# Kernel optimization log

Measured on AMD Instinct MI355X. Metric: run time of the kernel, lower is better.

## Reference

```python
import jax, jax.numpy as jnp
import numpy as np

N, D_IN, D_ATTN = 8192, 48, 8


def setup_inputs() -> dict:
    key = jax.random.key(0)
    ks = jax.random.split(key, 9)
    s = 1.0 / np.sqrt(D_IN)
    return {
        "x": jax.random.normal(ks[0], (N, D_IN), jnp.float32),
        "Kw": jax.random.normal(ks[1], (D_IN, D_ATTN), jnp.float32) * s,
        "Kb": jax.random.normal(ks[2], (D_ATTN,), jnp.float32) * s,
        "Qw": jax.random.normal(ks[3], (D_IN, D_ATTN), jnp.float32) * s,
        "Qb": jax.random.normal(ks[4], (D_ATTN,), jnp.float32) * s,
        "Vw": jax.random.normal(ks[5], (D_IN, D_ATTN), jnp.float32) * s,
        "Vb": jax.random.normal(ks[6], (D_ATTN,), jnp.float32) * s,
        "Zw": jax.random.normal(ks[7], (D_ATTN, D_IN), jnp.float32) * (1.0 / np.sqrt(D_ATTN)),
        "Zb": jax.random.normal(ks[8], (D_IN,), jnp.float32) * (1.0 / np.sqrt(D_ATTN)),
    }


def reference(x, Kw, Kb, Qw, Qb, Vw, Vb, Zw, Zb):
    # Tiny QKV projections: [N,48] -> [N,8]
    Xk = x @ Kw + Kb
    Xq = x @ Qw + Qb
    Xv = x @ Vw + Vb
    # Attention over the batch/row dimension: [N,8]@[8,N] -> [N,N]
    scale = jnp.sqrt(jnp.asarray(D_ATTN, jnp.float32))
    AM = jax.nn.softmax(Xk @ Xq.T / scale, axis=1)  # torch F.softmax 2D default dim=1
    Z = AM @ Xv                                      # [N,8]
    return x + (Z @ Zw + Zb)                         # residual + output proj [N,48]
```

## Files before the change

kernel.cpp:

```cpp
#include <hip/hip_runtime.h>
#include <hip/hip_fp16.h>


#define XKS_OFF  0
#define Q4_OFF   32768
#define VT_OFF   65536
#define KN2_OFF  102400
#define BMAX_OFF 110592
#define PART_OFF 110848

typedef _Float16 half8 __attribute__((ext_vector_type(8)));
typedef float f32x16 __attribute__((ext_vector_type(16)));
union U8 { unsigned u[4]; half8 h; };

static __device__ __forceinline__ unsigned pku(float a, float b) {
    auto t = __builtin_amdgcn_cvt_pkrtz(a, b);
    union { decltype(t) x; unsigned u; } c; c.x = t; return c.u;
}

__global__ __launch_bounds__(256) void proj_kernel(
    const float* __restrict__ x,
    const float* __restrict__ Kw, const float* __restrict__ Kb,
    const float* __restrict__ Qw, const float* __restrict__ Qb,
    const float* __restrict__ Vw, const float* __restrict__ Vb,
    unsigned* __restrict__ Xksf16, unsigned* __restrict__ Q4,
    unsigned* __restrict__ Vt, float* __restrict__ kn2,
    float* __restrict__ bmax)
{
    __shared__ float xs[32 * 49];
    __shared__ float wAll[3 * 388];
    __shared__ float bs[24];
    __shared__ float outv[32][25];
    const int tid = threadIdx.x;
    const int r0 = blockIdx.x * 32;

    for (int i = tid; i < 1536; i += 256) {
        int r = i / 48, c = i - r * 48;
        xs[r * 49 + c] = x[r0 * 48 + i];
    }
    for (int i = tid; i < 384; i += 256) {
        wAll[i]       = Kw[i];
        wAll[388 + i] = Qw[i];
        wAll[776 + i] = Vw[i];
    }
    if (tid < 8)       bs[tid] = Kb[tid];
    else if (tid < 16) bs[tid] = Qb[tid - 8];
    else if (tid < 24) bs[tid] = Vb[tid - 16];
    __syncthreads();

    const int rl = tid >> 3;
    const int g  = tid & 7;
    const int c0 = 3 * g;
    const float* xr = &xs[rl * 49];
    const float* w0 = &wAll[((c0 + 0) >> 3) * 388 + ((c0 + 0) & 7)];
    const float* w1 = &wAll[((c0 + 1) >> 3) * 388 + ((c0 + 1) & 7)];
    const float* w2 = &wAll[((c0 + 2) >> 3) * 388 + ((c0 + 2) & 7)];
    float a0 = bs[c0], a1 = bs[c0 + 1], a2 = bs[c0 + 2];
    #pragma unroll
    for (int k = 0; k < 48; k++) {
        const float xv = xr[k];
        a0 = fmaf(xv, w0[k * 8], a0);
        a1 = fmaf(xv, w1[k * 8], a1);
        a2 = fmaf(xv, w2[k * 8], a2);
    }
    outv[rl][c0] = a0; outv[rl][c0 + 1] = a1; outv[rl][c0 + 2] = a2;
    __syncthreads();

    const float kscale = 0.51008732149f;
    if (tid < 32) {
        uint4 o;
        o.x = pku(outv[tid][0] * kscale, outv[tid][1] * kscale);
        o.y = pku(outv[tid][2] * kscale, outv[tid][3] * kscale);
        o.z = pku(outv[tid][4] * kscale, outv[tid][5] * kscale);
        o.w = pku(outv[tid][6] * kscale, outv[tid][7] * kscale);
        ((uint4*)Xksf16)[r0 + tid] = o;
    } else if (tid < 64) {
        const int r = tid - 32;
        uint4 o;
        o.x = pku(outv[r][8],  outv[r][9]);
        o.y = pku(outv[r][10], outv[r][11]);
        o.z = pku(outv[r][12], outv[r][13]);
        o.w = pku(outv[r][14], outv[r][15]);
        ((uint4*)Q4)[r0 + r] = o;
    } else if (tid < 192) {
        const int i = tid - 64;
        const int c = i >> 4, t = i & 15;
        Vt[c * 4096 + blockIdx.x * 16 + t] =
            pku(outv[2 * t][16 + c], outv[2 * t + 1][16 + c]);
    } else if (tid < 224) {
        const int r = tid - 192;
        float n2 = 0.f;
        #pragma unroll
        for (int c = 0; c < 8; c++) n2 = fmaf(outv[r][8 + c], outv[r][8 + c], n2);
        #pragma unroll
        for (int off = 16; off > 0; off >>= 1)
            n2 = fmaxf(n2, __shfl_xor(n2, off, 64));
        if (r == 0) bmax[blockIdx.x] = n2;
    } else {
        const int r = tid - 224;
        float s = 0.f;
        #pragma unroll
        for (int c = 0; c < 8; c++) { const float v = outv[r][c]; s = fmaf(v, v, s); }
        kn2[r0 + r] = s * (kscale * kscale);
    }
    if (tid < 16)
        Vt[8 * 4096 + blockIdx.x * 16 + tid] = 0x3C003C00u;
}

__global__ __launch_bounds__(256) void attn_kernel(
    const uint4* __restrict__ Xks4, const uint4* __restrict__ Q4,
    const unsigned* __restrict__ Vt, const float* __restrict__ kn2,
    const float* __restrict__ bmax, float* __restrict__ part, int ntiles)
{
    const int tid  = threadIdx.x;
    const int lane = tid & 63;
    const int wv   = tid >> 6;
    const int wid  = blockIdx.x * 4 + wv;
    const int rg = wid & 255, ch = wid >> 8;
    const int h = lane >> 5, hl = lane & 31;
    const int rbase = rg * 32;
    const int j0base = ch * (ntiles * 32);

    float m = fmaxf(fmaxf(bmax[lane], bmax[64 + lane]),
                    fmaxf(bmax[128 + lane], bmax[192 + lane]));
    #pragma unroll
    for (int off = 32; off > 0; off >>= 1)
        m = fmaxf(m, __shfl_xor(m, off, 64));
    const float qmax2 = m;

    U8 Bk;
    if (h == 0) {
        const uint4 kv = Xks4[rbase + hl];
        Bk.u[0] = kv.x; Bk.u[1] = kv.y; Bk.u[2] = kv.z; Bk.u[3] = kv.w;
    } else {
        const float sinit = -sqrtf(kn2[rbase + hl] * qmax2);
        Bk.u[0] = pku(sinit, 0.f); Bk.u[1] = 0u; Bk.u[2] = 0u; Bk.u[3] = 0u;
    }

    const f32x16 zc = {0.f,0.f,0.f,0.f,0.f,0.f,0.f,0.f,
                       0.f,0.f,0.f,0.f,0.f,0.f,0.f,0.f};
    f32x16 acc = {0.f,0.f,0.f,0.f,0.f,0.f,0.f,0.f,
                  0.f,0.f,0.f,0.f,0.f,0.f,0.f,0.f};

    const int cva = hl < 9 ? hl : 8;
    const uint2* V2 = (const uint2*)Vt;
    const int u2base = cva * 2048 + h;

    int j0 = j0base;
    uint4 qv_n  = Q4[j0 + hl];
    uint2 va0_n = V2[u2base + (j0 >> 2) + 0];
    uint2 va1_n = V2[u2base + (j0 >> 2) + 2];
    uint2 va2_n = V2[u2base + (j0 >> 2) + 4];
    uint2 va3_n = V2[u2base + (j0 >> 2) + 6];

    for (int t = 0; t < ntiles; ++t) {
        const uint4 qv  = qv_n;
        const uint2 va0 = va0_n, va1 = va1_n, va2 = va2_n, va3 = va3_n;
        if (t + 1 < ntiles) {
            const int j1 = j0 + 32;
            qv_n  = Q4[j1 + hl];
            va0_n = V2[u2base + (j1 >> 2) + 0];
            va1_n = V2[u2base + (j1 >> 2) + 2];
            va2_n = V2[u2base + (j1 >> 2) + 4];
            va3_n = V2[u2base + (j1 >> 2) + 6];
        }

        U8 Aq;
        Aq.u[0] = h ? 0x00003C00u : qv.x;
        Aq.u[1] = h ? 0u : qv.y;
        Aq.u[2] = h ? 0u : qv.z;
        Aq.u[3] = h ? 0u : qv.w;
        const f32x16 s = __builtin_amdgcn_mfma_f32_32x32x16_f16(Aq.h, Bk.h, zc, 0, 0, 0);

        const unsigned pk01 = pku(__builtin_amdgcn_exp2f(s[0]),  __builtin_amdgcn_exp2f(s[1]));
        const unsigned pk23 = pku(__builtin_amdgcn_exp2f(s[2]),  __builtin_amdgcn_exp2f(s[3]));
        const unsigned pk45 = pku(__builtin_amdgcn_exp2f(s[4]),  __builtin_amdgcn_exp2f(s[5]));
        const unsigned pk67 = pku(__builtin_amdgcn_exp2f(s[6]),  __builtin_amdgcn_exp2f(s[7]));
        const unsigned pk89 = pku(__builtin_amdgcn_exp2f(s[8]),  __builtin_amdgcn_exp2f(s[9]));
        const unsigned pkAB = pku(__builtin_amdgcn_exp2f(s[10]), __builtin_amdgcn_exp2f(s[11]));
        const unsigned pkCD = pku(__builtin_amdgcn_exp2f(s[12]), __builtin_amdgcn_exp2f(s[13]));
        const unsigned pkEF = pku(__builtin_amdgcn_exp2f(s[14]), __builtin_amdgcn_exp2f(s[15]));

        U8 A2a; A2a.u[0] = va0.x; A2a.u[1] = va0.y; A2a.u[2] = va1.x; A2a.u[3] = va1.y;
        U8 B2a; B2a.u[0] = pk01;  B2a.u[1] = pk23;  B2a.u[2] = pk45;  B2a.u[3] = pk67;
        acc = __builtin_amdgcn_mfma_f32_32x32x16_f16(A2a.h, B2a.h, acc, 0, 0, 0);
        U8 A2b; A2b.u[0] = va2.x; A2b.u[1] = va2.y; A2b.u[2] = va3.x; A2b.u[3] = va3.y;
        U8 B2b; B2b.u[0] = pk89;  B2b.u[1] = pkAB;  B2b.u[2] = pkCD;  B2b.u[3] = pkEF;
        acc = __builtin_amdgcn_mfma_f32_32x32x16_f16(A2b.h, B2b.h, acc, 0, 0, 0);

        j0 += 32;
    }

    float* pr = part + ((size_t)ch * 8192 + rbase + hl) * 9;
    if (h == 0) {
        pr[0] = acc[0]; pr[1] = acc[1]; pr[2] = acc[2]; pr[3] = acc[3];
        pr[8] = acc[4];
    } else {
        pr[4] = acc[0]; pr[5] = acc[1]; pr[6] = acc[2]; pr[7] = acc[3];
    }
}

__global__ __launch_bounds__(256) void finish_kernel(
    const float* __restrict__ x,
    const float* __restrict__ Zw, const float* __restrict__ Zb,
    const float* __restrict__ part, float* __restrict__ out, int nch)
{
    __shared__ float Zs[32 * 9];
    __shared__ float Zl[32];
    __shared__ float zw_s[384];
    __shared__ float zb_s[48];
    const int tid = threadIdx.x;
    const int r0 = blockIdx.x * 32;

    for (int i = tid; i < 384; i += 256) zw_s[i] = Zw[i];
    if (tid < 48) zb_s[tid] = Zb[tid];

    {
        const int r = tid >> 3, c = tid & 7;
        float a = 0.f, l = 0.f;
        #pragma unroll 8
        for (int ch = 0; ch < nch; ch++) {
            const float* p = part + ((size_t)ch * 8192 + r0 + r) * 9;
            a += p[c];
            if (c == 0) l += p[8];
        }
        if (c == 0) Zl[r] = l;
        __syncthreads();
        Zs[r * 9 + c] = a * (1.0f / Zl[r]);
    }
    __syncthreads();

    for (int e = tid; e < 32 * 48; e += 256) {
        const int r = e / 48, c = e - r * 48;
        float o = x[r0 * 48 + e] + zb_s[c];
        #pragma unroll
        for (int k = 0; k < 8; k++) o = fmaf(Zs[r * 9 + k], zw_s[k * 48 + c], o);
        out[r0 * 48 + e] = o;
    }
}

extern "C" void kernel_launch(void* const* d_in, const int* in_sizes, int n_in,
                              void* d_out, int out_size, void* d_ws, size_t ws_size,
                              hipStream_t stream) {
    const float* x  = (const float*)d_in[0];
    const float* Kw = (const float*)d_in[1];
    const float* Kb = (const float*)d_in[2];
    const float* Qw = (const float*)d_in[3];
    const float* Qb = (const float*)d_in[4];
    const float* Vw = (const float*)d_in[5];
    const float* Vb = (const float*)d_in[6];
    const float* Zw = (const float*)d_in[7];
    const float* Zb = (const float*)d_in[8];
    float* out = (float*)d_out;

    float* ws = (float*)d_ws;
    unsigned* Xksf16 = (unsigned*)(ws + XKS_OFF);
    unsigned* Q4     = (unsigned*)(ws + Q4_OFF);
    unsigned* Vt     = (unsigned*)(ws + VT_OFF);
    float* kn2       = ws + KN2_OFF;
    float* bmax      = ws + BMAX_OFF;
    float* part      = ws + PART_OFF;

    int nch = 32;
    const size_t avail = ws_size / 4;
    while (nch > 1 && (size_t)PART_OFF + (size_t)nch * 8192 * 9 > avail) nch >>= 1;
    const int ntiles = 256 / nch;

    proj_kernel<<<256, 256, 0, stream>>>(x, Kw, Kb, Qw, Qb, Vw, Vb,
                                         Xksf16, Q4, Vt, kn2, bmax);
    attn_kernel<<<64 * nch, 256, 0, stream>>>((const uint4*)Xksf16,
                                              (const uint4*)Q4, Vt, kn2,
                                              bmax, part, ntiles);
    finish_kernel<<<256, 256, 0, stream>>>(x, Zw, Zb, part, out, nch);
}
```

Before: 111.9 us.

## Unroll attention tile loop and store partials row-major by chunk

Drops the manual one-tile register prefetch in the attention loop and adds an unroll-by-8 pragma instead, leaving the compiler to schedule loads across tiles. The partial-sum buffer is reordered so each row's chunk partials sit next to each other, which turns the finish kernel's reduction reads into contiguous accesses. The cost is that attention-kernel writes are now strided by nch*9 floats, and latency hiding now depends on how the compiler schedules the unrolled loop.

```diff
diff --git a/kernel.cpp b/kernel.cpp
--- a/kernel.cpp
+++ b/kernel.cpp
@@ -110,7 +110,8 @@
 __global__ __launch_bounds__(256) void attn_kernel(
     const uint4* __restrict__ Xks4, const uint4* __restrict__ Q4,
     const unsigned* __restrict__ Vt, const float* __restrict__ kn2,
-    const float* __restrict__ bmax, float* __restrict__ part, int ntiles)
+    const float* __restrict__ bmax, float* __restrict__ part,
+    int ntiles, int nch)
 {
     const int tid  = threadIdx.x;
     const int lane = tid & 63;
@@ -146,24 +147,15 @@
     const uint2* V2 = (const uint2*)Vt;
     const int u2base = cva * 2048 + h;
 
-    int j0 = j0base;
-    uint4 qv_n  = Q4[j0 + hl];
-    uint2 va0_n = V2[u2base + (j0 >> 2) + 0];
-    uint2 va1_n = V2[u2base + (j0 >> 2) + 2];
-    uint2 va2_n = V2[u2base + (j0 >> 2) + 4];
-    uint2 va3_n = V2[u2base + (j0 >> 2) + 6];
-
+    #pragma unroll 8
     for (int t = 0; t < ntiles; ++t) {
-        const uint4 qv  = qv_n;
-        const uint2 va0 = va0_n, va1 = va1_n, va2 = va2_n, va3 = va3_n;
-        if (t + 1 < ntiles) {
-            const int j1 = j0 + 32;
-            qv_n  = Q4[j1 + hl];
-            va0_n = V2[u2base + (j1 >> 2) + 0];
-            va1_n = V2[u2base + (j1 >> 2) + 2];
-            va2_n = V2[u2base + (j1 >> 2) + 4];
-            va3_n = V2[u2base + (j1 >> 2) + 6];
-        }
+        const int j0 = j0base + t * 32;
+
+        const uint4 qv  = Q4[j0 + hl];
+        const uint2 va0 = V2[u2base + (j0 >> 2) + 0];
+        const uint2 va1 = V2[u2base + (j0 >> 2) + 2];
+        const uint2 va2 = V2[u2base + (j0 >> 2) + 4];
+        const uint2 va3 = V2[u2base + (j0 >> 2) + 6];
 
         U8 Aq;
         Aq.u[0] = h ? 0x00003C00u : qv.x;
@@ -187,11 +179,9 @@
         U8 A2b; A2b.u[0] = va2.x; A2b.u[1] = va2.y; A2b.u[2] = va3.x; A2b.u[3] = va3.y;
         U8 B2b; B2b.u[0] = pk89;  B2b.u[1] = pkAB;  B2b.u[2] = pkCD;  B2b.u[3] = pkEF;
         acc = __builtin_amdgcn_mfma_f32_32x32x16_f16(A2b.h, B2b.h, acc, 0, 0, 0);
-
-        j0 += 32;
-    }
-
-    float* pr = part + ((size_t)ch * 8192 + rbase + hl) * 9;
+    }
+
+    float* pr = part + ((size_t)(rbase + hl) * nch + ch) * 9;
     if (h == 0) {
         pr[0] = acc[0]; pr[1] = acc[1]; pr[2] = acc[2]; pr[3] = acc[3];
         pr[8] = acc[4];
@@ -217,10 +207,11 @@
 
     {
         const int r = tid >> 3, c = tid & 7;
+        const float* base = part + (size_t)(r0 + r) * nch * 9;
         float a = 0.f, l = 0.f;
         #pragma unroll 8
         for (int ch = 0; ch < nch; ch++) {
-            const float* p = part + ((size_t)ch * 8192 + r0 + r) * 9;
+            const float* p = base + ch * 9;
             a += p[c];
             if (c == 0) l += p[8];
         }
@@ -270,6 +261,6 @@
                                          Xksf16, Q4, Vt, kn2, bmax);
     attn_kernel<<<64 * nch, 256, 0, stream>>>((const uint4*)Xksf16,
                                               (const uint4*)Q4, Vt, kn2,
-                                              bmax, part, ntiles);
+                                              bmax, part, ntiles, nch);
     finish_kernel<<<256, 256, 0, stream>>>(x, Zw, Zb, part, out, nch);
 }
```

New measurement: 112.1 us. Within noise of the previous version (+0.2%).
